# Performance work log

Measured on AMD Instinct MI355X. Metric: run time of the kernel, lower is better.

## Reference

```python
import jax, jax.numpy as jnp
import numpy as np

DEPTH = 6
GAMMA = 1e-4
DIM = 1024
HIDDEN = 16
OUT_DIM = 64
N = 16384


def setup_inputs() -> dict:
    key = jax.random.key(0)
    k0, k1, k2, k3, k4 = jax.random.split(key, 5)
    X = jax.random.normal(k0, (N, DIM), dtype=jnp.float32)
    s1 = 1.0 / np.sqrt(DIM)
    s2 = 1.0 / np.sqrt(HIDDEN)
    W1 = jax.random.uniform(k1, (DIM, HIDDEN), jnp.float32, -s1, s1)
    b1 = jax.random.uniform(k2, (HIDDEN,), jnp.float32, -s1, s1)
    W2 = jax.random.uniform(k3, (HIDDEN, OUT_DIM), jnp.float32, -s2, s2)
    b2 = jax.random.uniform(k4, (OUT_DIM,), jnp.float32, -s2, s2)
    return {"X": X, "W1": W1, "b1": b1, "W2": W2, "b2": b2}


def _mlp(X, W1, b1, W2, b2):
    # shared FeedForwardClassifier: Linear(dim,16) -> ReLU -> Linear(16,out_dim)
    return jax.nn.relu(X @ W1 + b1) @ W2 + b2


def reference(X, W1, b1, W2, b2):
    for _ in range(DEPTH):
        # custom LayerNorm: row-wise L2 normalization (no eps in original)
        Xn = X / jnp.linalg.norm(X, axis=-1, keepdims=True)  # [N, dim]
        P = jax.nn.softmax(_mlp(Xn, W1, b1, W2, b2), axis=-1)  # [N, out_dim]
        # X + g*P@P.T@X - g*X@X.T@X, contracted small-Gram-first (same math)
        PtX = P.T @ Xn          # [out_dim, dim]
        G = Xn.T @ Xn           # [dim, dim]
        X = Xn + GAMMA * (P @ PtX) - GAMMA * (Xn @ G)
    return _mlp(X, W1, b1, W2, b2)
```

## Files before the change

kernel.cpp:

```cpp
#include <hip/hip_runtime.h>


#define N_ROWS 16384
#define DIM 1024
#define HID 16
#define OUTD 64
#define DEPTH 6
#define GAMMA 1e-4f

typedef short bf16x8 __attribute__((ext_vector_type(8)));
typedef unsigned short u16x8 __attribute__((ext_vector_type(8)));
typedef float f32x4 __attribute__((ext_vector_type(4)));

#define AS1C(p) ((const __attribute__((address_space(1))) void*)(p))
#define AS3(p)  ((__attribute__((address_space(3))) void*)(p))

__device__ __forceinline__ unsigned short f2bf(float f) {
    unsigned u = __builtin_bit_cast(unsigned, f);
    u += 0x7fffu + ((u >> 16) & 1u);
    return (unsigned short)(u >> 16);
}
__device__ __forceinline__ float b2f(ushort u) {
    unsigned x = ((unsigned)u) << 16;
    return __builtin_bit_cast(float, x);
}
__device__ __forceinline__ int swz(int n, int row) {
    return (n & ~63) | ((((n >> 3) & 7) ^ (row & 7)) << 3) | (n & 7);
}

__global__ __launch_bounds__(256) void tobf16_k(const float* __restrict__ X,
        ushort* __restrict__ Xm, float* __restrict__ ssout) {
    int row = blockIdx.x, t = threadIdx.x;
    float4 v = ((const float4*)(X + (size_t)row * DIM))[t];
    ushort4 o4;
    o4.x = f2bf(v.x); o4.y = f2bf(v.y); o4.z = f2bf(v.z); o4.w = f2bf(v.w);
    *(ushort4*)(Xm + (size_t)row * DIM + swz(t * 4, row)) = o4;
    float ss = v.x * v.x + v.y * v.y + v.z * v.z + v.w * v.w;
    for (int o = 32; o > 0; o >>= 1) ss += __shfl_down(ss, o);
    __shared__ float wsum[4];
    if ((t & 63) == 0) wsum[t >> 6] = ss;
    __syncthreads();
    if (t == 0) ssout[row] = wsum[0] + wsum[1] + wsum[2] + wsum[3];
}

__device__ __forceinline__ void transpose_body(const ushort* __restrict__ Xm,
        const float* __restrict__ ss, ushort* __restrict__ XnT,
        int bx, int by, float* ts, float* riS) {
    int r0 = bx * 64;
    int c0 = by * 64;
    int t = threadIdx.x;
    if (t < 64) riS[t] = 1.0f / sqrtf(ss[r0 + t]);
    __syncthreads();
#pragma unroll
    for (int i = 0; i < 2; ++i) {
        int idx = i * 256 + t;
        int r = idx >> 3, lg = idx & 7;
        int rr = r0 + r;
        const ushort* p = Xm + (size_t)rr * DIM + c0 + ((lg ^ (rr & 7)) << 3);
        u16x8 a = *(const u16x8*)p;
        float s = riS[r];
        float* d = &ts[r * 65 + lg * 8];
#pragma unroll
        for (int u = 0; u < 8; ++u) d[u] = b2f(a[u]) * s;
    }
    __syncthreads();
#pragma unroll
    for (int i = 0; i < 2; ++i) {
        int g = i * 256 + t;
        int c = g >> 3;
        int rg = g & 7;
        u16x8 pk;
#pragma unroll
        for (int u = 0; u < 8; ++u) pk[u] = f2bf(ts[(rg * 8 + u) * 65 + c]);
        *(u16x8*)(XnT + (size_t)(c0 + c) * N_ROWS + r0 + ((rg ^ (c & 7)) << 3)) = pk;
    }
}

__device__ __forceinline__ void zgemm_body(const ushort* __restrict__ Xm,
        const ushort* __restrict__ W1T, const float* __restrict__ b1,
        float* __restrict__ z, const float* __restrict__ ss, int bidx) {
    int t = threadIdx.x;
    int wave = t >> 6, lane = t & 63;
    int rl = lane & 15, q = lane >> 4;
    int rowbase = bidx * 64 + wave * 16;
    int m = rowbase + rl;
    int msw = m & 7;
    const ushort* arow = Xm + (size_t)m * DIM;
    const ushort* brow = W1T + (size_t)rl * DIM + q * 8;
    f32x4 acc = {0.f, 0.f, 0.f, 0.f};
#pragma unroll 8
    for (int kt = 0; kt < DIM; kt += 32) {
        int gl = ((kt >> 3) & 7) | q;
        int off = (kt & ~63) + ((gl ^ msw) << 3);
        bf16x8 a = *(const bf16x8*)(arow + off);
        bf16x8 b = *(const bf16x8*)(brow + kt);
        acc = __builtin_amdgcn_mfma_f32_16x16x32_bf16(a, b, acc, 0, 0, 0);
    }
#pragma unroll
    for (int rg = 0; rg < 4; ++rg) {
        int mm = rowbase + q * 4 + rg;
        float s = ss ? 1.0f / sqrtf(ss[mm]) : 1.0f;
        z[(size_t)mm * HID + rl] = acc[rg] * s + b1[rl];
    }
}

__global__ __launch_bounds__(256) void txz_k(const ushort* __restrict__ Xm,
        const float* __restrict__ ss, ushort* __restrict__ XnT,
        const ushort* __restrict__ W1T, const float* __restrict__ b1,
        float* __restrict__ z) {
    __shared__ float ts[64 * 65];
    __shared__ float riS[64];
    int bid = blockIdx.x;
    if (bid < 4096) transpose_body(Xm, ss, XnT, bid & 255, bid >> 8, ts, riS);
    else            zgemm_body(Xm, W1T, b1, z, ss, bid - 4096);
}

__global__ __launch_bounds__(256) void transpose_k(const ushort* __restrict__ Xm,
        const float* __restrict__ ss, ushort* __restrict__ XnT) {
    __shared__ float ts[64 * 65];
    __shared__ float riS[64];
    transpose_body(Xm, ss, XnT, blockIdx.x, blockIdx.y, ts, riS);
}
__global__ __launch_bounds__(256) void zgemm_k(const ushort* __restrict__ Xm,
        const ushort* __restrict__ W1T, const float* __restrict__ b1,
        float* __restrict__ z, const float* __restrict__ ss) {
    zgemm_body(Xm, W1T, b1, z, ss, blockIdx.x);
}

__global__ __launch_bounds__(256) void prep_w1t_k(const float* __restrict__ W1,
        ushort* __restrict__ W1T) {
    int idx = blockIdx.x * 256 + threadIdx.x;
    int h = idx >> 10, j = idx & 1023;
    W1T[idx] = f2bf(W1[j * HID + h]);
}

__global__ __launch_bounds__(256) void head_k(const float* __restrict__ z,
        const float* __restrict__ W2, const float* __restrict__ b2,
        ushort* __restrict__ Pb, ushort* __restrict__ PTb,
        float* __restrict__ out, int do_softmax) {
    __shared__ float w2s[HID * OUTD];
    __shared__ float b2s[OUTD];
    int t = threadIdx.x;
    ((float4*)w2s)[t] = ((const float4*)W2)[t];
    if (t < OUTD) b2s[t] = b2[t];
    __syncthreads();
    int m = blockIdx.x * 256 + t;
    float h[HID];
    const float4* zp = (const float4*)(z + (size_t)m * HID);
#pragma unroll
    for (int i = 0; i < 4; ++i) {
        float4 v = zp[i];
        h[i * 4 + 0] = fmaxf(v.x, 0.f); h[i * 4 + 1] = fmaxf(v.y, 0.f);
        h[i * 4 + 2] = fmaxf(v.z, 0.f); h[i * 4 + 3] = fmaxf(v.w, 0.f);
    }
    float lo[OUTD];
#pragma unroll
    for (int o = 0; o < OUTD; ++o) lo[o] = b2s[o];
    for (int i = 0; i < HID; ++i) {
        float hv = h[i];
#pragma unroll
        for (int o = 0; o < OUTD; ++o) lo[o] += hv * w2s[i * OUTD + o];
    }
    if (do_softmax) {
        float mx = lo[0];
#pragma unroll
        for (int o = 1; o < OUTD; ++o) mx = fmaxf(mx, lo[o]);
        float sm = 0.f;
#pragma unroll
        for (int o = 0; o < OUTD; ++o) { float e = __expf(lo[o] - mx); lo[o] = e; sm += e; }
        float inv = 1.0f / sm;
#pragma unroll
        for (int o8 = 0; o8 < 8; ++o8) {
            u16x8 pk;
#pragma unroll
            for (int u = 0; u < 8; ++u) pk[u] = f2bf(lo[o8 * 8 + u] * inv);
            ((u16x8*)(Pb + (size_t)m * OUTD))[o8 ^ (m & 7)] = pk;
        }
#pragma unroll
        for (int o = 0; o < OUTD; ++o)
            PTb[(size_t)o * N_ROWS + swz(m, o)] = f2bf(lo[o] * inv);
    } else {
        float4* op = (float4*)(out + (size_t)m * OUTD);
#pragma unroll
        for (int o4 = 0; o4 < 16; ++o4) {
            float4 v; v.x = lo[o4 * 4 + 0]; v.y = lo[o4 * 4 + 1];
            v.z = lo[o4 * 4 + 2]; v.w = lo[o4 * 4 + 3];
            op[o4] = v;
        }
    }
}

__global__ __launch_bounds__(256) void reduce_k(const ushort* __restrict__ Gp,
        const ushort* __restrict__ PXp, ushort* __restrict__ Gsum,
        ushort* __restrict__ PXsum, int nzg, int nzp) {
    int idx = blockIdx.x * 256 + threadIdx.x;
    if (idx < 73728) {
        size_t off = (size_t)idx * 8;
        float acc[8] = {0.f, 0.f, 0.f, 0.f, 0.f, 0.f, 0.f, 0.f};
        for (int zz = 0; zz < nzg; ++zz) {
            u16x8 v = *(const u16x8*)(Gp + (size_t)zz * 589824 + off);
#pragma unroll
            for (int u = 0; u < 8; ++u) acc[u] += b2f(v[u]);
        }
        u16x8 o;
#pragma unroll
        for (int u = 0; u < 8; ++u) o[u] = f2bf(acc[u]);
        *(u16x8*)(Gsum + off) = o;
    } else {
        size_t off = (size_t)(idx - 73728) * 8;
        float acc[8] = {0.f, 0.f, 0.f, 0.f, 0.f, 0.f, 0.f, 0.f};
        for (int zz = 0; zz < nzp; ++zz) {
            u16x8 v = *(const u16x8*)(PXp + (size_t)zz * 65536 + off);
#pragma unroll
            for (int u = 0; u < 8; ++u) acc[u] += b2f(v[u]);
        }
        u16x8 o;
#pragma unroll
        for (int u = 0; u < 8; ++u) o[u] = f2bf(acc[u]);
        *(u16x8*)(PXsum + off) = o;
    }
}

__global__ __launch_bounds__(256) void castgp_k(const ushort* __restrict__ Gsum,
        const ushort* __restrict__ PXsum, ushort* __restrict__ Gb,
        ushort* __restrict__ PtXTb, float* __restrict__ ssz) {
    if (blockIdx.x < 64) ssz[blockIdx.x * 256 + threadIdx.x] = 0.f;
    int idx = blockIdx.x * 256 + threadIdx.x;
    if (idx < 262144) {
        int n = idx >> 8;
        int so = (idx & 255) * 4;
        int k0 = (so & ~63) | ((((so >> 3) & 7) ^ (n & 7)) << 3) | (so & 7);
        ushort po[4];
#pragma unroll
        for (int u = 0; u < 4; ++u) {
            int kk = k0 + u;
            int a = min(n, kk), b = max(n, kk);
            int tm = a >> 7, tn = b >> 7;
            int tlin = tm * 8 - ((tm * (tm - 1)) >> 1) + (tn - tm);
            size_t off = (size_t)tlin * 16384 + (size_t)(a & 127) * 128 + (b & 127);
            po[u] = (ushort)(Gsum[off] ^ 0x8000u);
        }
        ushort4 o; o.x = po[0]; o.y = po[1]; o.z = po[2]; o.w = po[3];
        *(ushort4*)(Gb + (size_t)n * DIM + so) = o;
    } else {
        int vv = idx - 262144;
        int d = vv >> 4;
        int so = (vv & 15) * 4;
        int k0 = ((((so >> 3) & 7) ^ (d & 7)) << 3) | (so & 7);
        const ushort* src = PXsum + (size_t)d * OUTD + k0;
        ushort4 o; o.x = src[0]; o.y = src[1]; o.z = src[2]; o.w = src[3];
        *(ushort4*)(PtXTb + (size_t)d * OUTD + so) = o;
    }
}

template<int BM, int BN, int EPI, int TRI>
__device__ __forceinline__ void gemm_body(
        const ushort* __restrict__ A0, int lda0,
        const ushort* __restrict__ B0, int ldb0, int k0len,
        const ushort* __restrict__ A1, int lda1,
        const ushort* __restrict__ B1, int ldb1, int k1len,
        float* __restrict__ C, int ldc,
        const float* __restrict__ ssrd, float gamma,
        float* __restrict__ ssacc, int pstride, int nz,
        int bx, int by, int bz, ushort* ls) {
    constexpr int WTN = BN / 2;
    constexpr int NF = WTN / 16;
    constexpr int NAW = BM / 64;
    constexpr int NBW = BN / 64;
    ushort* lsA = ls;
    ushort* lsB = ls + BM * 64;
    int t = threadIdx.x;
    int wave = t >> 6, lane = t & 63;
    int rl = lane & 15, q = lane >> 4;
    int wm = wave & 1, wn = wave >> 1;
    int m0, n0, zidx, tlin = 0;
    if (TRI) {
        int bid = bx;
        int bxx, tm = 0;
        if (nz == 16) {
            int rest = bid >> 3;
            bxx = rest % 36;
            int zhi = rest / 36;
            zidx = (bid & 7) | (zhi << 3);
        } else {
            zidx = bid & 3;
            bxx = bid >> 2;
        }
        tlin = bxx;
        while (bxx >= 8 - tm) { bxx -= 8 - tm; ++tm; }
        m0 = tm * 128; n0 = (tm + bxx) * 128;
    } else {
        m0 = bx * BM; n0 = by * BN; zidx = bz;
    }
    int lrow8 = lane >> 3, lgrp = lane & 7;
    bool isA = wave < NAW;
    bool active = wave < NAW + NBW;
    int wlocal = isA ? wave : wave - NAW;
    ushort* dstb = ls + (isA ? 0 : BM * 64) + wlocal * 4096;

    f32x4 acc[4][NF];
#pragma unroll
    for (int i = 0; i < 4; ++i)
#pragma unroll
        for (int j = 0; j < NF; ++j) acc[i][j] = f32x4{0.f, 0.f, 0.f, 0.f};
    float rvv[4][4];

    for (int seg = 0; seg < 2; ++seg) {
        int klen = seg ? k1len : k0len;
        if (klen > 0) {
            const ushort* OPA = seg ? A1 : A0;
            const ushort* OPB = seg ? B1 : B0;
            int ldaS = seg ? lda1 : lda0;
            int ldbS = seg ? ldb1 : ldb0;
            int kb = seg ? 0 : zidx * k0len;
            const ushort* srcb;
            size_t ldS;
            if (isA) {
                srcb = OPA + (size_t)(m0 + wlocal * 64 + lrow8) * ldaS + lgrp * 8;
                ldS = (size_t)ldaS;
            } else {
                srcb = OPB + (size_t)(n0 + wlocal * 64 + lrow8) * ldbS + lgrp * 8;
                ldS = (size_t)ldbS;
            }
            srcb += kb;
            for (int kt = 0; kt < klen; kt += 64) {
                if (active) {
#pragma unroll
                    for (int c = 0; c < 8; ++c)
                        __builtin_amdgcn_global_load_lds(AS1C(srcb + c * 8 * ldS),
                                                         AS3(dstb + c * 512), 16, 0, 0);
                    srcb += 64;
                }
                __syncthreads();
#pragma unroll
                for (int s = 0; s < 2; ++s) {
                    bf16x8 af[4], bfr[NF];
#pragma unroll
                    for (int i = 0; i < 4; ++i) {
                        int row = wm * 64 + i * 16 + rl;
                        int sg = ((s << 2) | q) ^ (row & 7);
                        af[i] = *(const bf16x8*)&lsA[row * 64 + sg * 8];
                    }
#pragma unroll
                    for (int j = 0; j < NF; ++j) {
                        int row = wn * WTN + j * 16 + rl;
                        int sg = ((s << 2) | q) ^ (row & 7);
                        bfr[j] = *(const bf16x8*)&lsB[row * 64 + sg * 8];
                    }
#pragma unroll
                    for (int i = 0; i < 4; ++i)
#pragma unroll
                        for (int j = 0; j < NF; ++j)
                            acc[i][j] = __builtin_amdgcn_mfma_f32_16x16x32_bf16(
                                af[i], bfr[j], acc[i][j], 0, 0, 0);
                }
                __syncthreads();
            }
        }
        if (EPI == 1 && seg == 0) {
#pragma unroll
            for (int i = 0; i < 4; ++i)
#pragma unroll
                for (int rg = 0; rg < 4; ++rg)
                    rvv[i][rg] = 1.0f / sqrtf(ssrd[m0 + wm * 64 + i * 16 + q * 4 + rg]);
#pragma unroll
            for (int i = 0; i < 4; ++i)
#pragma unroll
                for (int j = 0; j < NF; ++j)
#pragma unroll
                    for (int rg = 0; rg < 4; ++rg)
                        acc[i][j][rg] *= rvv[i][rg];
        }
    }

    if (EPI == 0) {
        ushort* Cb = (ushort*)C + (size_t)zidx * (size_t)pstride;
#pragma unroll
        for (int i = 0; i < 4; ++i)
#pragma unroll
            for (int j = 0; j < NF; ++j)
#pragma unroll
                for (int rg = 0; rg < 4; ++rg) {
                    float v = acc[i][j][rg];
                    float vp = __shfl_xor(v, 1);
                    if ((rl & 1) == 0) {
                        int ml = wm * 64 + i * 16 + q * 4 + rg;
                        int nl = wn * WTN + j * 16 + rl;
                        size_t off;
                        if (TRI)
                            off = (size_t)tlin * (BM * BN) + (size_t)ml * BN + nl;
                        else
                            off = (size_t)(m0 + ml) * ldc + (n0 + nl);
                        unsigned pk = (unsigned)f2bf(v) | ((unsigned)f2bf(vp) << 16);
                        *(unsigned*)(Cb + off) = pk;
                    }
                }
    } else {
#pragma unroll
        for (int i = 0; i < 4; ++i)
#pragma unroll
            for (int rg = 0; rg < 4; ++rg) {
                int m = m0 + wm * 64 + i * 16 + q * 4 + rg;
                float ssl = 0.f;
#pragma unroll
                for (int j = 0; j < NF; ++j) {
                    int n = n0 + wn * WTN + j * 16 + rl;
                    int so = swz(n, m);
                    float base = b2f(A0[(size_t)m * lda0 + so]);
                    float vf = base * rvv[i][rg] + gamma * acc[i][j][rg];
                    ((ushort*)C)[(size_t)m * ldc + so] = f2bf(vf);
                    ssl += vf * vf;
                }
                ssl += __shfl_xor(ssl, 1);
                ssl += __shfl_xor(ssl, 2);
                ssl += __shfl_xor(ssl, 4);
                ssl += __shfl_xor(ssl, 8);
                if (rl == 0) atomicAdd(&ssacc[m], ssl);
            }
    }
}

template<int BM, int BN, int EPI, int TRI>
__global__ __launch_bounds__(256, 3) void gemm_nt_k(
        const ushort* __restrict__ A0, int lda0,
        const ushort* __restrict__ B0, int ldb0, int k0len,
        const ushort* __restrict__ A1, int lda1,
        const ushort* __restrict__ B1, int ldb1, int k1len,
        float* __restrict__ C, int ldc,
        const float* __restrict__ ssrd, float gamma,
        float* __restrict__ ssacc, int pstride, int nz) {
    __shared__ ushort ls[(BM + BN) * 64];
    gemm_body<BM, BN, EPI, TRI>(A0, lda0, B0, ldb0, k0len, A1, lda1, B1, ldb1,
        k1len, C, ldc, ssrd, gamma, ssacc, pstride, nz,
        blockIdx.x, blockIdx.y, blockIdx.z, ls);
}

__global__ __launch_bounds__(256, 3) void gp_k(const ushort* __restrict__ XnT,
        const ushort* __restrict__ PTb, ushort* __restrict__ Gpart,
        ushort* __restrict__ PXpart) {
    __shared__ ushort ls[256 * 64];
    int bid = blockIdx.x;
    if (bid < 576) {
        gemm_body<128, 128, 0, 1>(XnT, N_ROWS, XnT, N_ROWS, 1024,
            nullptr, 0, nullptr, 0, 0,
            (float*)Gpart, 128, nullptr, 0.f, nullptr, 36 * 16384, 16,
            bid, 0, 0, ls);
    } else {
        int b2 = bid - 576;
        gemm_body<128, 64, 0, 0>(XnT, N_ROWS, PTb, N_ROWS, 512,
            nullptr, 0, nullptr, 0, 0,
            (float*)PXpart, OUTD, nullptr, 0.f, nullptr, DIM * OUTD, 0,
            b2 & 7, 0, b2 >> 3, ls);
    }
}

extern "C" void kernel_launch(void* const* d_in, const int* in_sizes, int n_in,
                              void* d_out, int out_size, void* d_ws, size_t ws_size,
                              hipStream_t stream) {
    const float* X = (const float*)d_in[0];
    const float* W1 = (const float*)d_in[1];
    const float* b1 = (const float*)d_in[2];
    const float* W2 = (const float*)d_in[3];
    const float* b2 = (const float*)d_in[4];
    float* out = (float*)d_out;
    char* ws = (char*)d_ws;

    constexpr size_t O_BufA    = 0;
    constexpr size_t O_BufB    = O_BufA + (size_t)N_ROWS * DIM * 2;
    constexpr size_t O_Pb      = O_BufB + (size_t)N_ROWS * DIM * 2;
    constexpr size_t O_PTb     = O_Pb + (size_t)N_ROWS * OUTD * 2;
    constexpr size_t O_Gb      = O_PTb + (size_t)OUTD * N_ROWS * 2;
    constexpr size_t O_PtXTb   = O_Gb + (size_t)DIM * DIM * 2;
    constexpr size_t O_ssB     = O_PtXTb + (size_t)DIM * OUTD * 2;
    constexpr size_t O_W1T     = O_ssB + (size_t)N_ROWS * 4;
    constexpr size_t O_ssA     = O_W1T + (size_t)HID * DIM * 2;
    constexpr size_t O_scratch = O_ssA + (size_t)N_ROWS * 4;
    constexpr size_t WS_BIG = O_scratch + (size_t)16 * 589824 * 2;

    ushort* bufA  = (ushort*)(ws + O_BufA);
    ushort* bufB  = (ushort*)(ws + O_BufB);
    ushort* Pb    = (ushort*)(ws + O_Pb);
    ushort* PTb   = (ushort*)(ws + O_PTb);
    ushort* Gb    = (ushort*)(ws + O_Gb);
    ushort* PtXTb = (ushort*)(ws + O_PtXTb);
    float*  ssB   = (float*)(ws + O_ssB);
    ushort* W1T   = (ushort*)(ws + O_W1T);
    float*  ssA   = (float*)(ws + O_ssA);
    float*  z     = (float*)(ws + O_scratch);
    ushort* Gpart = (ushort*)(ws + O_scratch);
    ushort* PXpart = (ushort*)d_out;
    ushort* Gsum  = PTb;
    ushort* PXsum = PTb + 589824;
    (void)in_sizes; (void)n_in; (void)out_size;

    const bool big = ws_size >= WS_BIG;
    const int nzg = big ? 16 : 4;
    const int nzp = big ? 32 : 8;

    prep_w1t_k<<<64, 256, 0, stream>>>(W1, W1T);
    tobf16_k<<<N_ROWS, 256, 0, stream>>>(X, bufA, ssA);

    ushort* xm  = bufA;
    ushort* alt = bufB;
    float* ssCur = ssA;
    float* ssNxt = ssB;

    for (int it = 0; it < DEPTH; ++it) {
        if (big) {
            txz_k<<<4096 + 256, 256, 0, stream>>>(xm, ssCur, alt, W1T, b1, z);
        } else {
            transpose_k<<<dim3(N_ROWS / 64, DIM / 64), 256, 0, stream>>>(xm, ssCur, alt);
            zgemm_k<<<N_ROWS / 64, 256, 0, stream>>>(xm, W1T, b1, z, ssCur);
        }
        head_k<<<N_ROWS / 256, 256, 0, stream>>>(z, W2, b2, Pb, PTb, nullptr, 1);
        if (big) {
            gp_k<<<576 + 256, 256, 0, stream>>>(alt, PTb, Gpart, PXpart);
        } else {
            gemm_nt_k<128, 128, 0, 1><<<dim3(36 * 4, 1, 1), 256, 0, stream>>>(
                alt, N_ROWS, alt, N_ROWS, 4096,
                nullptr, 0, nullptr, 0, 0,
                (float*)Gpart, 128, nullptr, 0.f, nullptr, 36 * 16384, 4);
            gemm_nt_k<128, 64, 0, 0><<<dim3(8, 1, 8), 256, 0, stream>>>(
                alt, N_ROWS, PTb, N_ROWS, 2048,
                nullptr, 0, nullptr, 0, 0,
                (float*)PXpart, OUTD, nullptr, 0.f, nullptr, DIM * OUTD, 0);
        }
        reduce_k<<<320, 256, 0, stream>>>(Gpart, PXpart, Gsum, PXsum, nzg, nzp);
        castgp_k<<<1088, 256, 0, stream>>>(Gsum, PXsum, Gb, PtXTb, ssNxt);
        gemm_nt_k<128, 128, 1, 0><<<dim3(N_ROWS / 128, DIM / 128, 1), 256, 0, stream>>>(
            xm, DIM, Gb, DIM, 1024,
            Pb, OUTD, PtXTb, OUTD, OUTD,
            (float*)alt, DIM, ssCur, GAMMA, ssNxt, 0, 0);
        ushort* tmp = xm; xm = alt; alt = tmp;
        float* ts2 = ssCur; ssCur = ssNxt; ssNxt = ts2;
    }

    zgemm_k<<<N_ROWS / 64, 256, 0, stream>>>(xm, W1T, b1, z, nullptr);
    head_k<<<N_ROWS / 256, 256, 0, stream>>>(z, W2, b2, Pb, PTb, out, 0);
}
```

Measured before the change: 908.7 us.

## Replace update GEMM with 256x256-tile, 8-wave ping-pong pipelined kernel

After: 971.2 us. +6.9%, slower.

```diff
diff --git a/kernel.cpp b/kernel.cpp
--- a/kernel.cpp
+++ b/kernel.cpp
@@ -454,6 +454,153 @@
     }
 }
 
+
+#define STG(OP, LD, ROW0, KCOL, DST, ISB, H) { \
+    _Pragma("unroll") for (int l_ = 0; l_ < 2; ++l_) { \
+        int flat_ = l_ * 512 + tid; \
+        int grp_ = flat_ & 7, rih_ = flat_ >> 3; \
+        int grow_ = (ISB) ? ((rih_ & 31) + (H) * 32 + (rih_ >> 5) * 64) \
+                          : ((rih_ & 63) + (H) * 64 + (rih_ >> 6) * 128); \
+        __builtin_amdgcn_global_load_lds( \
+            AS1C((OP) + (size_t)((ROW0) + grow_) * (LD) + (KCOL) \
+                 + ((grp_ ^ (grow_ & 7)) << 3)), \
+            AS3((DST) + flat_ * 8), 16, 0, 0); } }
+
+#define PHASE(BUF, MH, NH, STAGE_STMT, VM_STMT) { \
+    const ushort* lA_ = ls + (BUF) * 32768 + (MH) * 8192; \
+    const ushort* lB_ = ls + (BUF) * 32768 + 16384 + (NH) * 8192; \
+    bf16x8 af_[4][2], bf_[2][2]; \
+    _Pragma("unroll") for (int f_ = 0; f_ < 4; ++f_) \
+        _Pragma("unroll") for (int ks_ = 0; ks_ < 2; ++ks_) \
+            af_[f_][ks_] = *(const bf16x8*)&lA_[(wm2 * 64 + f_ * 16 + rl) * 64 \
+                + (((ks_ << 2) | q) ^ (rl & 7)) * 8]; \
+    _Pragma("unroll") for (int j_ = 0; j_ < 2; ++j_) \
+        _Pragma("unroll") for (int ks_ = 0; ks_ < 2; ++ks_) \
+            bf_[j_][ks_] = *(const bf16x8*)&lB_[(wn2 * 32 + j_ * 16 + rl) * 64 \
+                + (((ks_ << 2) | q) ^ (rl & 7)) * 8]; \
+    STAGE_STMT; \
+    __builtin_amdgcn_s_barrier(); \
+    asm volatile("s_waitcnt lgkmcnt(0)" ::: "memory"); \
+    __builtin_amdgcn_sched_barrier(0); \
+    __builtin_amdgcn_s_setprio(1); \
+    _Pragma("unroll") for (int f_ = 0; f_ < 4; ++f_) \
+        _Pragma("unroll") for (int j_ = 0; j_ < 2; ++j_) \
+            _Pragma("unroll") for (int ks_ = 0; ks_ < 2; ++ks_) \
+                acc[(MH) * 4 + f_][(NH) * 2 + j_] = \
+                    __builtin_amdgcn_mfma_f32_16x16x32_bf16(af_[f_][ks_], \
+                        bf_[j_][ks_], acc[(MH) * 4 + f_][(NH) * 2 + j_], 0, 0, 0); \
+    __builtin_amdgcn_s_setprio(0); \
+    VM_STMT; \
+    __builtin_amdgcn_s_barrier(); }
+
+__global__ __launch_bounds__(512, 1) void upd_k(
+        const ushort* __restrict__ Xm, const ushort* __restrict__ Gb,
+        const ushort* __restrict__ Pb, const ushort* __restrict__ PtXTb,
+        ushort* __restrict__ Cm, const float* __restrict__ ssrd,
+        float gamma, float* __restrict__ ssacc) {
+    __shared__ ushort ls[65536];
+    int tid = threadIdx.x;
+    int wave = tid >> 6, lane = tid & 63;
+    int rl = lane & 15, q = lane >> 4;
+    int wm2 = wave >> 2, wn2 = wave & 3;
+    int m0 = blockIdx.x * 256, n0 = blockIdx.y * 256;
+
+    f32x4 acc[8][4];
+#pragma unroll
+    for (int i = 0; i < 8; ++i)
+#pragma unroll
+        for (int j = 0; j < 4; ++j) acc[i][j] = f32x4{0.f, 0.f, 0.f, 0.f};
+
+    STG(Xm, DIM, m0, 0,  ls,                 0, 0);
+    STG(Gb, DIM, n0, 0,  ls + 16384,         1, 0);
+    STG(Xm, DIM, m0, 0,  ls + 8192,          0, 1);
+    STG(Gb, DIM, n0, 0,  ls + 24576,         1, 1);
+    STG(Xm, DIM, m0, 64, ls + 32768,         0, 0);
+    STG(Gb, DIM, n0, 64, ls + 49152,         1, 0);
+    asm volatile("s_waitcnt vmcnt(0)" ::: "memory");
+    __builtin_amdgcn_s_barrier();
+
+#pragma unroll 1
+    for (int it = 0; it < 8; ++it) {
+        int k1 = (2 * it + 1) * 64;
+        int k2 = (2 * it + 2) * 64;
+        int k3 = (2 * it + 3) * 64;
+        bool pf = (it < 7);
+        PHASE(0, 0, 0, STG(Xm, DIM, m0, k1, ls + 40960, 0, 1), );
+        PHASE(0, 0, 1, STG(Gb, DIM, n0, k1, ls + 57344, 1, 1), );
+        PHASE(0, 1, 0, if (pf) STG(Xm, DIM, m0, k2, ls, 0, 0), );
+        PHASE(0, 1, 1, if (pf) STG(Gb, DIM, n0, k2, ls + 16384, 1, 0),
+              if (pf) { asm volatile("s_waitcnt vmcnt(4)" ::: "memory"); }
+              else    { asm volatile("s_waitcnt vmcnt(0)" ::: "memory"); });
+        PHASE(1, 0, 0, if (pf) STG(Xm, DIM, m0, k2, ls + 8192, 0, 1), );
+        PHASE(1, 0, 1, if (pf) STG(Gb, DIM, n0, k2, ls + 24576, 1, 1), );
+        PHASE(1, 1, 0, if (pf) STG(Xm, DIM, m0, k3, ls + 32768, 0, 0), );
+        PHASE(1, 1, 1, if (pf) STG(Gb, DIM, n0, k3, ls + 49152, 1, 0),
+              if (pf) { asm volatile("s_waitcnt vmcnt(4)" ::: "memory"); }
+              else    { asm volatile("s_waitcnt vmcnt(0)" ::: "memory"); });
+    }
+
+    STG(Pb,    OUTD, m0, 0, ls,         0, 0);
+    STG(Pb,    OUTD, m0, 0, ls + 8192,  0, 1);
+    STG(PtXTb, OUTD, n0, 0, ls + 16384, 1, 0);
+    STG(PtXTb, OUTD, n0, 0, ls + 24576, 1, 1);
+
+    float rvv[8][4];
+#pragma unroll
+    for (int i = 0; i < 8; ++i)
+#pragma unroll
+        for (int rg = 0; rg < 4; ++rg) {
+            rvv[i][rg] = 1.0f / sqrtf(ssrd[m0 + wm2 * 128 + i * 16 + q * 4 + rg]);
+#pragma unroll
+            for (int j = 0; j < 4; ++j) acc[i][j][rg] *= rvv[i][rg];
+        }
+    __syncthreads();
+
+#pragma unroll
+    for (int mh = 0; mh < 2; ++mh)
+#pragma unroll
+        for (int nh = 0; nh < 2; ++nh) {
+            const ushort* lA_ = ls + mh * 8192;
+            const ushort* lB_ = ls + 16384 + nh * 8192;
+#pragma unroll
+            for (int f = 0; f < 4; ++f)
+#pragma unroll
+                for (int j = 0; j < 2; ++j)
+#pragma unroll
+                    for (int ks = 0; ks < 2; ++ks) {
+                        bf16x8 a8 = *(const bf16x8*)&lA_[(wm2 * 64 + f * 16 + rl) * 64
+                            + (((ks << 2) | q) ^ (rl & 7)) * 8];
+                        bf16x8 b8 = *(const bf16x8*)&lB_[(wn2 * 32 + j * 16 + rl) * 64
+                            + (((ks << 2) | q) ^ (rl & 7)) * 8];
+                        acc[mh * 4 + f][nh * 2 + j] =
+                            __builtin_amdgcn_mfma_f32_16x16x32_bf16(a8, b8,
+                                acc[mh * 4 + f][nh * 2 + j], 0, 0, 0);
+                    }
+        }
+
+#pragma unroll
+    for (int i = 0; i < 8; ++i)
+#pragma unroll
+        for (int rg = 0; rg < 4; ++rg) {
+            int m = m0 + wm2 * 128 + i * 16 + q * 4 + rg;
+            float ssl = 0.f;
+#pragma unroll
+            for (int j = 0; j < 4; ++j) {
+                int n = n0 + wn2 * 64 + j * 16 + rl;
+                int so = swz(n, m);
+                float base = b2f(Xm[(size_t)m * DIM + so]);
+                float vf = base * rvv[i][rg] + gamma * acc[i][j][rg];
+                Cm[(size_t)m * DIM + so] = f2bf(vf);
+                ssl += vf * vf;
+            }
+            ssl += __shfl_xor(ssl, 1);
+            ssl += __shfl_xor(ssl, 2);
+            ssl += __shfl_xor(ssl, 4);
+            ssl += __shfl_xor(ssl, 8);
+            if (rl == 0) atomicAdd(&ssacc[m], ssl);
+        }
+}
+
 extern "C" void kernel_launch(void* const* d_in, const int* in_sizes, int n_in,
                               void* d_out, int out_size, void* d_ws, size_t ws_size,
                               hipStream_t stream) {
@@ -527,10 +674,8 @@
         }
         reduce_k<<<320, 256, 0, stream>>>(Gpart, PXpart, Gsum, PXsum, nzg, nzp);
         castgp_k<<<1088, 256, 0, stream>>>(Gsum, PXsum, Gb, PtXTb, ssNxt);
-        gemm_nt_k<128, 128, 1, 0><<<dim3(N_ROWS / 128, DIM / 128, 1), 256, 0, stream>>>(
-            xm, DIM, Gb, DIM, 1024,
-            Pb, OUTD, PtXTb, OUTD, OUTD,
-            (float*)alt, DIM, ssCur, GAMMA, ssNxt, 0, 0);
+        upd_k<<<dim3(N_ROWS / 256, DIM / 256, 1), 512, 0, stream>>>(
+            xm, Gb, Pb, PtXTb, alt, ssCur, GAMMA, ssNxt);
         ushort* tmp = xm; xm = alt; alt = tmp;
         float* ts2 = ssCur; ssCur = ssNxt; ssNxt = ts2;
     }
```
